# Performance work log

Hardware: AMD Instinct MI355X
Metric: run time of the kernel (lower is better)

## Reference

```python
import jax, jax.numpy as jnp
import numpy as np

B, S, E, D, DE = 8, 128, 50, 300, 50  # batch, seq, edge_dim, gcn_dim, dep_embed_dim
EPS = 1e-6


def setup_inputs() -> dict:
    key = jax.random.key(0)
    ks = jax.random.split(key, 9)
    weight_prob_softmax = jax.nn.softmax(jax.random.normal(ks[0], (B, S, S, E)), axis=2)
    weight_adj = jax.random.normal(ks[1], (B, S, S, E))
    gcn_inputs = jax.random.normal(ks[2], (B, S, D))
    # self-loop added to adjacency after permute -> [B, E, S, S]; identity loops
    self_loop = jnp.broadcast_to(jnp.eye(S, dtype=jnp.float32), (B, E, S, S))
    W_w = jax.random.normal(ks[3], (D, D)) * 0.05          # gcn linear (in, out)
    W_b = jnp.zeros((D,))
    ln_a = jnp.ones((D,))
    ln_b = jnp.zeros((D,))
    refine_W = jax.random.normal(ks[4], (2 * D + 3 * E, DE)) * 0.05  # (750, 50)
    refine_b = jnp.zeros((DE,))
    return {
        "weight_prob_softmax": weight_prob_softmax,
        "weight_adj": weight_adj,
        "gcn_inputs": gcn_inputs,
        "self_loop": self_loop,
        "W_w": W_w, "W_b": W_b,
        "ln_a": ln_a, "ln_b": ln_b,
        "refine_W": refine_W, "refine_b": refine_b,
    }


def reference(weight_prob_softmax, weight_adj, gcn_inputs, self_loop,
              W_w, W_b, ln_a, ln_b, refine_W, refine_b):
    b, s, d = gcn_inputs.shape
    e = weight_prob_softmax.shape[-1]
    # [B,S,S,E] -> [B,E,S,S], add self loops
    wps = jnp.transpose(weight_prob_softmax, (0, 3, 1, 2)) + self_loop
    # per-relation-channel message passing: Ax[b,e,i,:] = sum_j wps[b,e,i,j] * x[b,j,:]
    Ax = jnp.einsum('beij,bjd->beid', wps, gcn_inputs)
    Ax = Ax.mean(axis=1)  # avg pooling over edge channels -> [B,S,D]
    h = Ax @ W_w + W_b
    # LayerNorm with unbiased std (torch x.std default) and (std + eps)
    mean = h.mean(axis=-1, keepdims=True)
    var_unbiased = jnp.sum((h - mean) ** 2, axis=-1, keepdims=True) / (d - 1)
    std = jnp.sqrt(var_unbiased)
    h = ln_a * (h - mean) / (std + EPS) + ln_b
    node = jax.nn.relu(h)  # [B,S,D]
    # node1[b,i,j] = node[b,j]; node2[b,i,j] = node[b,i]
    node1 = jnp.broadcast_to(node[:, None, :, :], (b, s, s, d))
    node2 = jnp.broadcast_to(node[:, :, None, :], (b, s, s, d))
    # diagonal edge features: [B,E,S] -> [B,S,E]
    diag = jnp.transpose(jnp.diagonal(weight_adj, axis1=1, axis2=2), (0, 2, 1))
    edge_i = jnp.broadcast_to(diag[:, None, :, :], (b, s, s, e))  # edge_i[b,i,j]=diag[b,j]
    edge_j = jnp.broadcast_to(diag[:, :, None, :], (b, s, s, e))  # edge_j[b,i,j]=diag[b,i]
    feat = jnp.concatenate([weight_adj, edge_i, edge_j, node1, node2], axis=-1)
    edge_out = feat @ refine_W + refine_b  # [B,S,S,DE]
    return node, edge_out
```

## Files before the change

kernel.cpp:

```cpp
#include <hip/hip_runtime.h>
#include <hip/hip_bf16.h>


typedef __bf16 bf16x8 __attribute__((ext_vector_type(8)));
typedef float f32x4 __attribute__((ext_vector_type(4)));

__device__ __forceinline__ unsigned short f2bf(float f) {
    __hip_bfloat16 h = __float2bfloat16(f);
    union { __hip_bfloat16 h; unsigned short u; } c; c.h = h; return c.u;
}

__global__ void __launch_bounds__(1024) k_node(
    const float* __restrict__ wps,
    const float* __restrict__ wa,
    const float* __restrict__ x,
    const float* __restrict__ Ww,
    const float* __restrict__ Wb,
    const float* __restrict__ lna,
    const float* __restrict__ lnb,
    const float* __restrict__ Rw,
    const float* __restrict__ rb,
    float* __restrict__ node_out,
    float* __restrict__ R1, float* __restrict__ R2)
{
    __shared__ __align__(16) float axp[4864];
    __shared__ __align__(16) float axm4[1216];
    __shared__ __align__(16) float Mlt[512];
    __shared__ __align__(16) float srcL[1408];
    __shared__ float red1[20], red2[20], stats[8];

    int tid = threadIdx.x;
    int g = tid >> 8, t = tid & 255;
    int row0 = blockIdx.x * 4;
    int b = row0 >> 7, i0 = row0 & 127;

    {
        int idx = tid & 511;
        int h = tid >> 9;
        int r = idx >> 7, j = idx & 127;
        const float2* p = (const float2*)(wps + ((size_t)(row0 + r) * 128 + j) * 50);
        float s = 0.f;
        if (h == 0) {
#pragma unroll
            for (int n = 0; n < 13; ++n) { float2 v = p[n]; s += v.x + v.y; }
        } else {
#pragma unroll
            for (int n = 13; n < 25; ++n) { float2 v = p[n]; s += v.x + v.y; }
        }
        axp[tid] = s;
    }
    __syncthreads();
    if (tid < 512) {
        int r = tid >> 7, j = tid & 127;
        float s = axp[tid] + axp[tid + 512];
        Mlt[j * 4 + r] = s * (1.0f / 50.0f) + (((i0 + r) == j) ? 1.0f : 0.0f);
    } else if (tid < 712) {
        int idx = tid - 512, r = idx / 50, e = idx % 50;
        srcL[e * 4 + r] = wa[((size_t)(row0 + r) * 128 + (i0 + r)) * 50 + e];
    }
    __syncthreads();

    int d0 = t;
    bool has2 = (t < 44);
    int d1 = has2 ? 256 + t : 299;

    {
        f32x4 a0 = {0.f, 0.f, 0.f, 0.f}, a1 = {0.f, 0.f, 0.f, 0.f};
        const float* xp = x + (size_t)b * 38400;
        int j0 = g * 32;
#pragma unroll 8
        for (int jj = 0; jj < 32; ++jj) {
            int j = j0 + jj;
            f32x4 m4 = *(const f32x4*)&Mlt[j * 4];
            float xv0 = xp[j * 300 + d0];
            float xv1 = xp[j * 300 + d1];
            a0 += m4 * xv0;
            a1 += m4 * xv1;
        }
        *(f32x4*)&axp[d0 * 16 + g * 4] = a0;
        if (has2) *(f32x4*)&axp[d1 * 16 + g * 4] = a1;
    }
    __syncthreads();
    if (tid < 304) {
        f32x4 s = {0.f, 0.f, 0.f, 0.f};
        if (tid < 300)
            s = *(f32x4*)&axp[tid * 16]     + *(f32x4*)&axp[tid * 16 + 4]
              + *(f32x4*)&axp[tid * 16 + 8] + *(f32x4*)&axp[tid * 16 + 12];
        *(f32x4*)&axm4[tid * 4] = s;
    }
    __syncthreads();

    {
        f32x4 h0 = {0.f, 0.f, 0.f, 0.f}, h1 = {0.f, 0.f, 0.f, 0.f};
        int kb = g * 76, ke = (g == 3) ? 300 : g * 76 + 76;
#pragma unroll 4
        for (int k = kb; k < ke; ++k) {
            f32x4 m4 = *(const f32x4*)&axm4[k * 4];
            float w0 = Ww[k * 300 + d0];
            float w1 = Ww[k * 300 + d1];
            h0 += m4 * w0;
            h1 += m4 * w1;
        }
        *(f32x4*)&axp[d0 * 16 + g * 4] = h0;
        if (has2) *(f32x4*)&axp[d1 * 16 + g * 4] = h1;
    }
    __syncthreads();

    f32x4 hv = {0.f, 0.f, 0.f, 0.f};
    int wv = tid >> 6, lane = tid & 63;
    if (tid < 320) {
        if (tid < 300) {
            hv = *(f32x4*)&axp[tid * 16]     + *(f32x4*)&axp[tid * 16 + 4]
               + *(f32x4*)&axp[tid * 16 + 8] + *(f32x4*)&axp[tid * 16 + 12];
            hv += Wb[tid];
        }
        float s1r[4], s2r[4];
#pragma unroll
        for (int r = 0; r < 4; ++r) { s1r[r] = hv[r]; s2r[r] = hv[r] * hv[r]; }
        for (int off = 32; off; off >>= 1) {
#pragma unroll
            for (int r = 0; r < 4; ++r) {
                s1r[r] += __shfl_down(s1r[r], off);
                s2r[r] += __shfl_down(s2r[r], off);
            }
        }
        if (lane == 0) {
#pragma unroll
            for (int r = 0; r < 4; ++r) { red1[wv * 4 + r] = s1r[r]; red2[wv * 4 + r] = s2r[r]; }
        }
    }
    __syncthreads();
    if (tid < 4) {
        float s1 = 0.f, s2 = 0.f;
#pragma unroll
        for (int w = 0; w < 5; ++w) { s1 += red1[w * 4 + tid]; s2 += red2[w * 4 + tid]; }
        float mean = s1 * (1.0f / 300.0f);
        float var = (s2 - 300.0f * mean * mean) * (1.0f / 299.0f);
        var = fmaxf(var, 0.0f);
        stats[tid * 2] = mean;
        stats[tid * 2 + 1] = 1.0f / (sqrtf(var) + 1e-6f);
    }
    __syncthreads();

    if (tid < 300) {
        float la = lna[tid], lb = lnb[tid];
        f32x4 nv;
#pragma unroll
        for (int r = 0; r < 4; ++r) {
            float v = la * (hv[r] - stats[r * 2]) * stats[r * 2 + 1] + lb;
            v = fmaxf(v, 0.f);
            nv[r] = v;
            node_out[(size_t)(row0 + r) * 300 + tid] = v;
        }
        *(f32x4*)&srcL[(50 + tid) * 4] = nv;
    }
    __syncthreads();

    if (tid < 500) {
        int p = tid / 50, k = tid % 50;
        f32x4 r1a = {0.f, 0.f, 0.f, 0.f}, r2a = {0.f, 0.f, 0.f, 0.f};
        int ib = p * 35;
#pragma unroll 5
        for (int idx = ib; idx < ib + 35; ++idx) {
            f32x4 sv = *(const f32x4*)&srcL[idx * 4];
            float w1, w2;
            if (idx < 50) { w1 = Rw[(50 + idx) * 50 + k]; w2 = Rw[(100 + idx) * 50 + k]; }
            else { int d = idx - 50; w1 = Rw[(150 + d) * 50 + k]; w2 = Rw[(450 + d) * 50 + k]; }
            r1a += sv * w1;
            r2a += sv * w2;
        }
        *(f32x4*)&axp[(p * 50 + k) * 4] = r1a;
        *(f32x4*)&axp[2000 + (p * 50 + k) * 4] = r2a;
    }
    __syncthreads();
    if (tid < 200) {
        int r = tid / 50, k = tid % 50;
        float s1 = 0.f, s2 = rb[k];
#pragma unroll
        for (int p = 0; p < 10; ++p) {
            s1 += axp[(p * 50 + k) * 4 + r];
            s2 += axp[2000 + (p * 50 + k) * 4 + r];
        }
        R1[(size_t)(row0 + r) * 50 + k] = s1;
        R2[(size_t)(row0 + r) * 50 + k] = s2;
    }
}

__global__ void __launch_bounds__(256) k_edge(
    const float* __restrict__ wa,
    const float* __restrict__ Rw,
    const float* __restrict__ R1, const float* __restrict__ R2,
    float* __restrict__ eout)
{
    __shared__ __align__(16) unsigned char smem[27648];
    unsigned short* waA  = (unsigned short*)smem;
    unsigned short* rwBT = (unsigned short*)(smem + 18432);
    float* outF = (float*)smem;
    int tid = threadIdx.x;
    int bi = blockIdx.x;
    int b = bi >> 7;

    for (int idx = tid; idx < 2304; idx += 256) ((unsigned int*)rwBT)[idx] = 0u;
    for (int idx = tid; idx < 1408; idx += 256) {
        int j = idx / 11, c = idx % 11;
        *((unsigned int*)(waA + j * 72 + 50) + c) = 0u;
    }
    __syncthreads();

    const float2* wap = (const float2*)(wa + (size_t)bi * 6400);
    for (int idx = tid; idx < 3200; idx += 256) {
        float2 v = wap[idx];
        int f = idx * 2;
        int j = f / 50, e = f % 50;
        unsigned int pack = (unsigned int)f2bf(v.x) | ((unsigned int)f2bf(v.y) << 16);
        *(unsigned int*)(waA + j * 72 + e) = pack;
    }
    for (int idx = tid; idx < 2500; idx += 256) {
        int e = idx / 50, kk = idx % 50;
        rwBT[kk * 72 + e] = f2bf(Rw[idx]);
    }
    __syncthreads();

    int lane = tid & 63, wv = tid >> 6;
    int q = lane >> 4, lr = lane & 15;
    f32x4 acc[2][4] = {};

#pragma unroll
    for (int ks = 0; ks < 2; ++ks) {
        int e0 = ks * 32 + q * 8;
        bf16x8 a0 = *(const bf16x8*)&waA[(wv * 32 + lr) * 72 + e0];
        bf16x8 a1 = *(const bf16x8*)&waA[(wv * 32 + 16 + lr) * 72 + e0];
#pragma unroll
        for (int nt = 0; nt < 4; ++nt) {
            bf16x8 bb = *(const bf16x8*)&rwBT[(nt * 16 + lr) * 72 + e0];
            acc[0][nt] = __builtin_amdgcn_mfma_f32_16x16x32_bf16(a0, bb, acc[0][nt], 0, 0, 0);
            acc[1][nt] = __builtin_amdgcn_mfma_f32_16x16x32_bf16(a1, bb, acc[1][nt], 0, 0, 0);
        }
    }
    __syncthreads();

    const float* r2p = R2 + (size_t)bi * 50;
#pragma unroll
    for (int nt = 0; nt < 4; ++nt) {
        int kk = nt * 16 + lr;
        if (kk < 50) {
            float r2v = r2p[kk];
#pragma unroll
            for (int mi = 0; mi < 2; ++mi) {
                int jbase = wv * 32 + mi * 16 + q * 4;
#pragma unroll
                for (int r = 0; r < 4; ++r)
                    outF[(jbase + r) * 50 + kk] = acc[mi][nt][r] + r2v;
            }
        }
    }
    __syncthreads();

    const float4* R1b = (const float4*)(R1 + (size_t)b * 6400);
    const float4* L4  = (const float4*)outF;
    float4* op4 = (float4*)(eout + (size_t)bi * 6400);
    for (int f4 = tid; f4 < 1600; f4 += 256) {
        float4 v = L4[f4];
        float4 r = R1b[f4];
        v.x += r.x; v.y += r.y; v.z += r.z; v.w += r.w;
        op4[f4] = v;
    }
}

extern "C" void kernel_launch(void* const* d_in, const int* in_sizes, int n_in,
                              void* d_out, int out_size, void* d_ws, size_t ws_size,
                              hipStream_t stream)
{
    const float* wps = (const float*)d_in[0];
    const float* wa  = (const float*)d_in[1];
    const float* x   = (const float*)d_in[2];
    const float* Ww  = (const float*)d_in[4];
    const float* Wb  = (const float*)d_in[5];
    const float* lna = (const float*)d_in[6];
    const float* lnb = (const float*)d_in[7];
    const float* Rw  = (const float*)d_in[8];
    const float* rb  = (const float*)d_in[9];

    float* R1 = (float*)d_ws;
    float* R2 = ((float*)d_ws) + 51200;

    float* node_out = (float*)d_out;
    float* edge_out = node_out + 307200;

    k_node<<<256, 1024, 0, stream>>>(wps, wa, x, Ww, Wb, lna, lnb, Rw, rb,
                                     node_out, R1, R2);
    k_edge<<<1024, 256, 0, stream>>>(wa, Rw, R1, R2, edge_out);
}
```

Baseline: 156.7 us.

## Process two rows per block in node kernel with 512 blocks of 512 threads

The node kernel now handles two sequence rows per block instead of four, launching 512 blocks of 512 threads rather than 256 blocks of 1024. Each thread now covers three output columns with 2-wide accumulators, and the shared buffers shrink to match. The aim is to fill more of the GPU's compute units and cut per-block latency. The cost is that x and Ww are re-read from global memory by twice as many blocks, since each block reuses them across only two rows.

```diff
diff --git a/kernel.cpp b/kernel.cpp
--- a/kernel.cpp
+++ b/kernel.cpp
@@ -4,13 +4,14 @@
 
 typedef __bf16 bf16x8 __attribute__((ext_vector_type(8)));
 typedef float f32x4 __attribute__((ext_vector_type(4)));
+typedef float f32x2 __attribute__((ext_vector_type(2)));
 
 __device__ __forceinline__ unsigned short f2bf(float f) {
     __hip_bfloat16 h = __float2bfloat16(f);
     union { __hip_bfloat16 h; unsigned short u; } c; c.h = h; return c.u;
 }
 
-__global__ void __launch_bounds__(1024) k_node(
+__global__ void __launch_bounds__(512) k_node(
     const float* __restrict__ wps,
     const float* __restrict__ wa,
     const float* __restrict__ x,
@@ -23,117 +24,119 @@
     float* __restrict__ node_out,
     float* __restrict__ R1, float* __restrict__ R2)
 {
-    __shared__ __align__(16) float axp[4864];
-    __shared__ __align__(16) float axm4[1216];
-    __shared__ __align__(16) float Mlt[512];
-    __shared__ __align__(16) float srcL[1408];
-    __shared__ float red1[20], red2[20], stats[8];
+    __shared__ __align__(16) float axp[2432];
+    __shared__ __align__(16) float axm2[608];
+    __shared__ __align__(16) float Mlt[256];
+    __shared__ __align__(16) float srcL[704];
+    __shared__ float red1[10], red2[10], stats[4];
 
     int tid = threadIdx.x;
-    int g = tid >> 8, t = tid & 255;
-    int row0 = blockIdx.x * 4;
+    int row0 = blockIdx.x * 2;
     int b = row0 >> 7, i0 = row0 & 127;
 
     {
-        int idx = tid & 511;
-        int h = tid >> 9;
-        int r = idx >> 7, j = idx & 127;
-        const float2* p = (const float2*)(wps + ((size_t)(row0 + r) * 128 + j) * 50);
+        int p = tid & 255, h = tid >> 8;
+        int r = p >> 7, j = p & 127;
+        const float2* pp = (const float2*)(wps + ((size_t)(row0 + r) * 128 + j) * 50);
         float s = 0.f;
         if (h == 0) {
 #pragma unroll
-            for (int n = 0; n < 13; ++n) { float2 v = p[n]; s += v.x + v.y; }
+            for (int n = 0; n < 13; ++n) { float2 v = pp[n]; s += v.x + v.y; }
         } else {
 #pragma unroll
-            for (int n = 13; n < 25; ++n) { float2 v = p[n]; s += v.x + v.y; }
+            for (int n = 13; n < 25; ++n) { float2 v = pp[n]; s += v.x + v.y; }
         }
         axp[tid] = s;
     }
     __syncthreads();
-    if (tid < 512) {
+    if (tid < 256) {
         int r = tid >> 7, j = tid & 127;
-        float s = axp[tid] + axp[tid + 512];
-        Mlt[j * 4 + r] = s * (1.0f / 50.0f) + (((i0 + r) == j) ? 1.0f : 0.0f);
-    } else if (tid < 712) {
-        int idx = tid - 512, r = idx / 50, e = idx % 50;
-        srcL[e * 4 + r] = wa[((size_t)(row0 + r) * 128 + (i0 + r)) * 50 + e];
-    }
-    __syncthreads();
-
-    int d0 = t;
-    bool has2 = (t < 44);
-    int d1 = has2 ? 256 + t : 299;
+        float s = axp[tid] + axp[tid + 256];
+        Mlt[j * 2 + r] = s * (1.0f / 50.0f) + (((i0 + r) == j) ? 1.0f : 0.0f);
+    } else if (tid < 356) {
+        int idx = tid - 256, r = idx / 50, e = idx % 50;
+        srcL[e * 2 + r] = wa[((size_t)(row0 + r) * 128 + (i0 + r)) * 50 + e];
+    }
+    __syncthreads();
+
+    int t = tid & 127, g = tid >> 7;
+    bool has3 = (t < 44);
+    int d2 = has3 ? 256 + t : 299;
 
     {
-        f32x4 a0 = {0.f, 0.f, 0.f, 0.f}, a1 = {0.f, 0.f, 0.f, 0.f};
+        f32x2 a0 = {0.f, 0.f}, a1 = {0.f, 0.f}, a2 = {0.f, 0.f};
         const float* xp = x + (size_t)b * 38400;
         int j0 = g * 32;
 #pragma unroll 8
         for (int jj = 0; jj < 32; ++jj) {
             int j = j0 + jj;
-            f32x4 m4 = *(const f32x4*)&Mlt[j * 4];
-            float xv0 = xp[j * 300 + d0];
-            float xv1 = xp[j * 300 + d1];
-            a0 += m4 * xv0;
-            a1 += m4 * xv1;
-        }
-        *(f32x4*)&axp[d0 * 16 + g * 4] = a0;
-        if (has2) *(f32x4*)&axp[d1 * 16 + g * 4] = a1;
-    }
-    __syncthreads();
-    if (tid < 304) {
-        f32x4 s = {0.f, 0.f, 0.f, 0.f};
-        if (tid < 300)
-            s = *(f32x4*)&axp[tid * 16]     + *(f32x4*)&axp[tid * 16 + 4]
-              + *(f32x4*)&axp[tid * 16 + 8] + *(f32x4*)&axp[tid * 16 + 12];
-        *(f32x4*)&axm4[tid * 4] = s;
+            f32x2 m2 = *(const f32x2*)&Mlt[j * 2];
+            float xv0 = xp[j * 300 + t];
+            float xv1 = xp[j * 300 + 128 + t];
+            float xv2 = xp[j * 300 + d2];
+            a0 += m2 * xv0;
+            a1 += m2 * xv1;
+            a2 += m2 * xv2;
+        }
+        *(f32x2*)&axp[t * 8 + g * 2] = a0;
+        *(f32x2*)&axp[(128 + t) * 8 + g * 2] = a1;
+        if (has3) *(f32x2*)&axp[(256 + t) * 8 + g * 2] = a2;
+    }
+    __syncthreads();
+    if (tid < 300) {
+        f32x2 s = *(f32x2*)&axp[tid * 8]     + *(f32x2*)&axp[tid * 8 + 2]
+                + *(f32x2*)&axp[tid * 8 + 4] + *(f32x2*)&axp[tid * 8 + 6];
+        *(f32x2*)&axm2[tid * 2] = s;
     }
     __syncthreads();
 
     {
-        f32x4 h0 = {0.f, 0.f, 0.f, 0.f}, h1 = {0.f, 0.f, 0.f, 0.f};
-        int kb = g * 76, ke = (g == 3) ? 300 : g * 76 + 76;
+        f32x2 h0 = {0.f, 0.f}, h1 = {0.f, 0.f}, h2 = {0.f, 0.f};
+        int kb = g * 75, ke = kb + 75;
 #pragma unroll 4
         for (int k = kb; k < ke; ++k) {
-            f32x4 m4 = *(const f32x4*)&axm4[k * 4];
-            float w0 = Ww[k * 300 + d0];
-            float w1 = Ww[k * 300 + d1];
-            h0 += m4 * w0;
-            h1 += m4 * w1;
-        }
-        *(f32x4*)&axp[d0 * 16 + g * 4] = h0;
-        if (has2) *(f32x4*)&axp[d1 * 16 + g * 4] = h1;
-    }
-    __syncthreads();
-
-    f32x4 hv = {0.f, 0.f, 0.f, 0.f};
+            f32x2 m2 = *(const f32x2*)&axm2[k * 2];
+            float w0 = Ww[k * 300 + t];
+            float w1 = Ww[k * 300 + 128 + t];
+            float w2 = Ww[k * 300 + d2];
+            h0 += m2 * w0;
+            h1 += m2 * w1;
+            h2 += m2 * w2;
+        }
+        *(f32x2*)&axp[t * 8 + g * 2] = h0;
+        *(f32x2*)&axp[(128 + t) * 8 + g * 2] = h1;
+        if (has3) *(f32x2*)&axp[(256 + t) * 8 + g * 2] = h2;
+    }
+    __syncthreads();
+
+    f32x2 hv = {0.f, 0.f};
     int wv = tid >> 6, lane = tid & 63;
     if (tid < 320) {
         if (tid < 300) {
-            hv = *(f32x4*)&axp[tid * 16]     + *(f32x4*)&axp[tid * 16 + 4]
-               + *(f32x4*)&axp[tid * 16 + 8] + *(f32x4*)&axp[tid * 16 + 12];
+            hv = *(f32x2*)&axp[tid * 8]     + *(f32x2*)&axp[tid * 8 + 2]
+               + *(f32x2*)&axp[tid * 8 + 4] + *(f32x2*)&axp[tid * 8 + 6];
             hv += Wb[tid];
         }
-        float s1r[4], s2r[4];
-#pragma unroll
-        for (int r = 0; r < 4; ++r) { s1r[r] = hv[r]; s2r[r] = hv[r] * hv[r]; }
+        float s1r[2], s2r[2];
+#pragma unroll
+        for (int r = 0; r < 2; ++r) { s1r[r] = hv[r]; s2r[r] = hv[r] * hv[r]; }
         for (int off = 32; off; off >>= 1) {
 #pragma unroll
-            for (int r = 0; r < 4; ++r) {
+            for (int r = 0; r < 2; ++r) {
                 s1r[r] += __shfl_down(s1r[r], off);
                 s2r[r] += __shfl_down(s2r[r], off);
             }
         }
         if (lane == 0) {
 #pragma unroll
-            for (int r = 0; r < 4; ++r) { red1[wv * 4 + r] = s1r[r]; red2[wv * 4 + r] = s2r[r]; }
-        }
-    }
-    __syncthreads();
-    if (tid < 4) {
+            for (int r = 0; r < 2; ++r) { red1[wv * 2 + r] = s1r[r]; red2[wv * 2 + r] = s2r[r]; }
+        }
+    }
+    __syncthreads();
+    if (tid < 2) {
         float s1 = 0.f, s2 = 0.f;
 #pragma unroll
-        for (int w = 0; w < 5; ++w) { s1 += red1[w * 4 + tid]; s2 += red2[w * 4 + tid]; }
+        for (int w = 0; w < 5; ++w) { s1 += red1[w * 2 + tid]; s2 += red2[w * 2 + tid]; }
         float mean = s1 * (1.0f / 300.0f);
         float var = (s2 - 300.0f * mean * mean) * (1.0f / 299.0f);
         var = fmaxf(var, 0.0f);
@@ -144,42 +147,42 @@
 
     if (tid < 300) {
         float la = lna[tid], lb = lnb[tid];
-        f32x4 nv;
-#pragma unroll
-        for (int r = 0; r < 4; ++r) {
+        f32x2 nv;
+#pragma unroll
+        for (int r = 0; r < 2; ++r) {
             float v = la * (hv[r] - stats[r * 2]) * stats[r * 2 + 1] + lb;
             v = fmaxf(v, 0.f);
             nv[r] = v;
             node_out[(size_t)(row0 + r) * 300 + tid] = v;
         }
-        *(f32x4*)&srcL[(50 + tid) * 4] = nv;
+        *(f32x2*)&srcL[(50 + tid) * 2] = nv;
     }
     __syncthreads();
 
     if (tid < 500) {
         int p = tid / 50, k = tid % 50;
-        f32x4 r1a = {0.f, 0.f, 0.f, 0.f}, r2a = {0.f, 0.f, 0.f, 0.f};
+        f32x2 r1a = {0.f, 0.f}, r2a = {0.f, 0.f};
         int ib = p * 35;
 #pragma unroll 5
         for (int idx = ib; idx < ib + 35; ++idx) {
-            f32x4 sv = *(const f32x4*)&srcL[idx * 4];
+            f32x2 sv = *(const f32x2*)&srcL[idx * 2];
             float w1, w2;
             if (idx < 50) { w1 = Rw[(50 + idx) * 50 + k]; w2 = Rw[(100 + idx) * 50 + k]; }
             else { int d = idx - 50; w1 = Rw[(150 + d) * 50 + k]; w2 = Rw[(450 + d) * 50 + k]; }
             r1a += sv * w1;
             r2a += sv * w2;
         }
-        *(f32x4*)&axp[(p * 50 + k) * 4] = r1a;
-        *(f32x4*)&axp[2000 + (p * 50 + k) * 4] = r2a;
-    }
-    __syncthreads();
-    if (tid < 200) {
+        *(f32x2*)&axp[(p * 50 + k) * 2] = r1a;
+        *(f32x2*)&axp[1024 + (p * 50 + k) * 2] = r2a;
+    }
+    __syncthreads();
+    if (tid < 100) {
         int r = tid / 50, k = tid % 50;
         float s1 = 0.f, s2 = rb[k];
 #pragma unroll
         for (int p = 0; p < 10; ++p) {
-            s1 += axp[(p * 50 + k) * 4 + r];
-            s2 += axp[2000 + (p * 50 + k) * 4 + r];
+            s1 += axp[(p * 50 + k) * 2 + r];
+            s2 += axp[1024 + (p * 50 + k) * 2 + r];
         }
         R1[(size_t)(row0 + r) * 50 + k] = s1;
         R2[(size_t)(row0 + r) * 50 + k] = s2;
@@ -287,7 +290,7 @@
     float* node_out = (float*)d_out;
     float* edge_out = node_out + 307200;
 
-    k_node<<<256, 1024, 0, stream>>>(wps, wa, x, Ww, Wb, lna, lnb, Rw, rb,
-                                     node_out, R1, R2);
+    k_node<<<512, 512, 0, stream>>>(wps, wa, x, Ww, Wb, lna, lnb, Rw, rb,
+                                    node_out, R1, R2);
     k_edge<<<1024, 256, 0, stream>>>(wa, Rw, R1, R2, edge_out);
 }
```

After: 162.0 us. 3.4% more time.
